# Kernel tuning notes

Measured on AMD Instinct MI355X. Metric: run time of the kernel, lower is better.

The kernel has to match this reference:

```python
import jax, jax.numpy as jnp
import numpy as np
import math

B, T, D, H = 128, 512, 512, 512


def setup_inputs() -> dict:
    key = jax.random.key(0)
    ks = jax.random.split(key, 6)
    s = 1.0 / math.sqrt(H)
    return {
        "values": jax.random.normal(ks[0], (B, T, D), jnp.float32),
        "Deltas": jax.random.uniform(ks[1], (B, T, D), jnp.float32),
        "W_att": jax.random.normal(ks[2], (D, D), jnp.float32) * s,
        "b_att": jnp.zeros((D,), jnp.float32),
        "W_ih": jax.random.normal(ks[3], (4 * H, D), jnp.float32) * s,
        "W_hh": jax.random.normal(ks[4], (4 * H, H), jnp.float32) * s,
        "b_ih": jnp.zeros((4 * H,), jnp.float32),
        "b_hh": jnp.zeros((4 * H,), jnp.float32),
    }


def lstm_cell(x, h, c, W_ih, W_hh, b_ih, b_hh):
    # torch.nn.LSTMCell: gates ordered i, f, g, o
    g = x @ W_ih.T + b_ih + h @ W_hh.T + b_hh
    i, f, gg, o = jnp.split(g, 4, axis=-1)
    c2 = jax.nn.sigmoid(f) * c + jax.nn.sigmoid(i) * jnp.tanh(gg)
    h2 = jax.nn.sigmoid(o) * jnp.tanh(c2)
    return h2, c2


def reference(values, Deltas, W_att, b_att, W_ih, W_hh, b_ih, b_hh):
    Bn, Tn, Dn = values.shape
    Hn = W_hh.shape[1]
    # cumsum over time then reverse along time (reverse_tensor)
    Del = jnp.flip(jnp.cumsum(Deltas, axis=-2), axis=1)  # [B,T,D]
    v_att = values @ W_att.T + b_att                      # attn-projected inputs [B,T,D]
    # a_ij = bmm(atten_linear(values), values^T) -> [B,T,T]
    a_ij = jnp.einsum('btd,bsd->bts', v_att, values)
    h0 = jnp.zeros((Bn, Hn), values.dtype)
    c0 = jnp.zeros((Bn, Hn), values.dtype)

    def step(carry, x_t):
        h, c = carry
        h2, c2 = lstm_cell(x_t, h, c, W_ih, W_hh, b_ih, b_hh)
        return (h2, c2), (h2, c2)

    xs = jnp.swapaxes(v_att[:, :-1], 0, 1)  # [T-1, B, D]
    (h_last, _), (hs, cs) = jax.lax.scan(step, (h0, c0), xs)
    hs = jnp.swapaxes(hs, 0, 1)  # [B, T-1, H]
    cs = jnp.swapaxes(cs, 0, 1)  # [B, T-1, H]

    # attention-weighted cell-state mixing for the final step
    alpha = jax.nn.softmax(a_ij[:, -1, :-1], axis=-1)[..., None]  # [B,T-1,1]
    d = Del[:, 1:]                                                # [B,T-1,D]
    C_i = jnp.sum(alpha * cs / jnp.log(math.e + d), axis=1)       # [B,H]

    hT, cT = lstm_cell(v_att[:, -1], h_last, C_i, W_ih, W_hh, b_ih, b_hh)
    h_n = jnp.concatenate([hs, hT[:, None, :]], axis=1)  # [B,T,H]
    return h_n
```

## Files before the change

kernel.cpp:

```cpp
#include <hip/hip_runtime.h>
#include <cstdint>

#define DEVI __device__ __forceinline__

typedef unsigned short ushort_t;
typedef __attribute__((ext_vector_type(8))) short s16x8;
typedef __attribute__((ext_vector_type(4))) int i32x4;
typedef __attribute__((ext_vector_type(4))) float f32x4;

DEVI ushort_t f2bf(float f) {
  uint32_t u = __builtin_bit_cast(uint32_t, f);
  u += 0x7fffu + ((u >> 16) & 1u);
  return (ushort_t)(u >> 16);
}
DEVI float bf2f(ushort_t u) {
  uint32_t x = ((uint32_t)u) << 16;
  return __builtin_bit_cast(float, x);
}
DEVI float sigmoidf_(float x) { return 1.0f / (1.0f + __expf(-x)); }
DEVI float tanhf_(float x) {
  float e = __expf(-2.0f * fabsf(x));
  float r = (1.0f - e) / (1.0f + e);
  return copysignf(r, x);
}

DEVI void load_tag16(i32x4& dst, const uint32_t* p) {
  asm volatile("global_load_dwordx4 %0, %1, off sc0 sc1" : "=v"(dst) : "v"(p));
}
DEVI void store_tagged(uint32_t* p, uint32_t v) {
  asm volatile("global_store_dword %0, %1, off sc0 sc1" :: "v"(p), "v"(v) : "memory");
}
DEVI void wait_vm0() { asm volatile("s_waitcnt vmcnt(0)" ::: "memory"); }

__global__ void cast_kernel(const float* __restrict__ in, ushort_t* __restrict__ out, long n) {
  long i = ((long)blockIdx.x * blockDim.x + threadIdx.x) * 8;
  if (i >= n) return;
  float4 a = *(const float4*)(in + i);
  float4 b = *(const float4*)(in + i + 4);
  union { s16x8 v; ushort_t u[8]; } r;
  r.u[0] = f2bf(a.x); r.u[1] = f2bf(a.y); r.u[2] = f2bf(a.z); r.u[3] = f2bf(a.w);
  r.u[4] = f2bf(b.x); r.u[5] = f2bf(b.y); r.u[6] = f2bf(b.z); r.u[7] = f2bf(b.w);
  *(s16x8*)(out + i) = r.v;
}

__global__ void transpose512(const float* __restrict__ in, float* __restrict__ out) {
  __shared__ float tile[32][33];
  int bx = blockIdx.x * 32, by = blockIdx.y * 32;
  int tx = threadIdx.x, ty = threadIdx.y;
  for (int i = 0; i < 32; i += 8)
    tile[ty + i][tx] = in[(by + ty + i) * 512 + bx + tx];
  __syncthreads();
  for (int i = 0; i < 32; i += 8)
    out[(bx + ty + i) * 512 + by + tx] = tile[tx][ty + i];
}

__global__ __launch_bounds__(256, 2)
void gemm_bt(const ushort_t* __restrict__ A, const ushort_t* __restrict__ B,
             const float* __restrict__ bias0, const float* __restrict__ bias1,
             ushort_t* __restrict__ C, int N, int K) {
  __shared__ __align__(16) ushort_t As[128 * 64];
  __shared__ __align__(16) ushort_t Bs[128 * 64];
  const int tid = threadIdx.x;
  const int lane = tid & 63, wv = tid >> 6;
  const int wm = wv >> 1, wn = wv & 1;
  const int l15 = lane & 15, l4 = lane >> 4;
  const long m0 = (long)blockIdx.x * 128;
  const int n0 = blockIdx.y * 128;
  const int nkt = K / 64;

  f32x4 acc[4][4] = {};

  int soff[4];
#pragma unroll
  for (int i = 0; i < 4; ++i) {
    int c = tid + i * 256;
    int r = c >> 3, ks = c & 7;
    soff[i] = r * 64 + ((ks ^ (r & 7)) << 3);
  }

#pragma unroll
  for (int i = 0; i < 4; ++i) {
    int c = tid + i * 256; int r = c >> 3; int ks = c & 7;
    *(s16x8*)&As[soff[i]] = *(const s16x8*)&A[(m0 + r) * K + ks * 8];
    *(s16x8*)&Bs[soff[i]] = *(const s16x8*)&B[(long)(n0 + r) * K + ks * 8];
  }
  __syncthreads();

  for (int kt = 0; kt < nkt; ++kt) {
    s16x8 ra[4], rb[4];
    const bool more = (kt + 1 < nkt);
    if (more) {
      const long kb = (long)(kt + 1) * 64;
#pragma unroll
      for (int i = 0; i < 4; ++i) {
        int c = tid + i * 256; int r = c >> 3; int ks = c & 7;
        ra[i] = *(const s16x8*)&A[(m0 + r) * K + kb + ks * 8];
        rb[i] = *(const s16x8*)&B[(long)(n0 + r) * K + kb + ks * 8];
      }
    }
#pragma unroll
    for (int kk = 0; kk < 2; ++kk) {
      s16x8 af[4], bfv[4];
      int slot = kk * 4 + l4;
#pragma unroll
      for (int i = 0; i < 4; ++i) {
        int rA = wm * 64 + i * 16 + l15;
        af[i] = *(const s16x8*)&As[rA * 64 + ((slot ^ (rA & 7)) << 3)];
        int rB = wn * 64 + i * 16 + l15;
        bfv[i] = *(const s16x8*)&Bs[rB * 64 + ((slot ^ (rB & 7)) << 3)];
      }
#pragma unroll
      for (int i = 0; i < 4; ++i)
#pragma unroll
        for (int j = 0; j < 4; ++j)
          acc[i][j] = __builtin_amdgcn_mfma_f32_16x16x32_bf16(af[i], bfv[j], acc[i][j], 0, 0, 0);
    }
    __syncthreads();
    if (more) {
#pragma unroll
      for (int i = 0; i < 4; ++i) {
        *(s16x8*)&As[soff[i]] = ra[i];
        *(s16x8*)&Bs[soff[i]] = rb[i];
      }
      __syncthreads();
    }
  }
#pragma unroll
  for (int i = 0; i < 4; ++i) {
#pragma unroll
    for (int j = 0; j < 4; ++j) {
#pragma unroll
      for (int r = 0; r < 4; ++r) {
        long m = m0 + wm * 64 + i * 16 + l4 * 4 + r;
        int n = n0 + wn * 64 + j * 16 + l15;
        float v = acc[i][j][r];
        if (bias0) v += bias0[n];
        if (bias1) v += bias1[n];
        C[m * (long)N + n] = f2bf(v);
      }
    }
  }
}

__global__ void bias_combo_kernel(const float* __restrict__ W_ih, const float* __restrict__ b_att,
                                  const float* __restrict__ b_ih, const float* __restrict__ b_hh,
                                  float* __restrict__ bc) {
  int n = blockIdx.x * 256 + threadIdx.x;
  __shared__ float ba[512];
  for (int k = threadIdx.x; k < 512; k += 256) ba[k] = b_att[k];
  __syncthreads();
  float s = b_ih[n] + b_hh[n];
  const float* row = W_ih + (long)n * 512;
  for (int k = 0; k < 512; ++k) s += row[k] * ba[k];
  bc[n] = s;
}

__global__ void vT_kernel(const float* __restrict__ values, const float* __restrict__ W_attT,
                          const float* __restrict__ b_att, float* __restrict__ vT) {
  int b = blockIdx.y;
  int n = blockIdx.x * 256 + threadIdx.x;
  __shared__ float xr[512];
  const float* row = values + ((long)b * 512 + 511) * 512;
  for (int k = threadIdx.x; k < 512; k += 256) xr[k] = row[k];
  __syncthreads();
  float acc = b_att[n];
  for (int k = 0; k < 512; ++k) acc += xr[k] * W_attT[k * 512 + n];
  vT[b * 512 + n] = acc;
}

__global__ void dtot_kernel(const float* __restrict__ Deltas, float* __restrict__ Dtot) {
  int idx = blockIdx.x * 256 + threadIdx.x;
  int b = idx >> 9, ch = idx & 511;
  const float* p = Deltas + (long)b * 512 * 512 + ch;
  float s = 0.0f;
  for (int t = 0; t < 511; ++t) s += p[(long)t * 512];
  Dtot[idx] = s;
}

__global__ void logits_kernel(const float* __restrict__ values, const float* __restrict__ vT,
                              float* __restrict__ logits) {
  int b = blockIdx.y;
  int wave = threadIdx.x >> 6, lane = threadIdx.x & 63;
  float vreg[8];
  const float* vtb = vT + b * 512;
#pragma unroll
  for (int j = 0; j < 8; ++j) vreg[j] = vtb[lane * 8 + j];
  int s0 = blockIdx.x * 64 + wave * 16;
  for (int si = 0; si < 16; ++si) {
    int s = s0 + si;
    if (s >= 511) break;
    const float* row = values + ((long)b * 512 + s) * 512 + lane * 8;
    float4 a = *(const float4*)row;
    float4 c = *(const float4*)(row + 4);
    float d = a.x * vreg[0] + a.y * vreg[1] + a.z * vreg[2] + a.w * vreg[3] +
              c.x * vreg[4] + c.y * vreg[5] + c.z * vreg[6] + c.w * vreg[7];
#pragma unroll
    for (int off = 32; off; off >>= 1) d += __shfl_xor(d, off);
    if (lane == 0) logits[b * 512 + s] = d;
  }
}

__global__ void softmax_kernel(float* __restrict__ logits) {
  int b = blockIdx.x, tid = threadIdx.x;
  __shared__ float wmax[4], wsum[4];
  float v0 = (tid < 511) ? logits[b * 512 + tid] : -1e30f;
  float v1 = (tid + 256 < 511) ? logits[b * 512 + tid + 256] : -1e30f;
  float m = fmaxf(v0, v1);
#pragma unroll
  for (int off = 32; off; off >>= 1) m = fmaxf(m, __shfl_xor(m, off));
  if ((tid & 63) == 0) wmax[tid >> 6] = m;
  __syncthreads();
  m = fmaxf(fmaxf(wmax[0], wmax[1]), fmaxf(wmax[2], wmax[3]));
  float e0 = (tid < 511) ? __expf(v0 - m) : 0.0f;
  float e1 = (tid + 256 < 511) ? __expf(v1 - m) : 0.0f;
  float s = e0 + e1;
#pragma unroll
  for (int off = 32; off; off >>= 1) s += __shfl_xor(s, off);
  if ((tid & 63) == 0) wsum[tid >> 6] = s;
  __syncthreads();
  s = wsum[0] + wsum[1] + wsum[2] + wsum[3];
  float inv = 1.0f / s;
  __syncthreads();
  if (tid < 511) logits[b * 512 + tid] = e0 * inv;
  if (tid + 256 < 511) logits[b * 512 + tid + 256] = e1 * inv;
}

__global__ __launch_bounds__(256, 1)
void scan_kernel(const float* __restrict__ W_hh, const ushort_t* __restrict__ Gx,
                 const float* __restrict__ alpha, const float* __restrict__ Dtot,
                 const float* __restrict__ Deltas, uint32_t* __restrict__ hbuf32,
                 float* __restrict__ out) {
  __shared__ __align__(16) ushort_t whh[64 * 512];
  __shared__ float gbuf[2][4][4][16][16];
  const int tid = threadIdx.x;
  const int bg = blockIdx.x & 7, hc = blockIdx.x >> 3;
  const int b0 = bg * 16, n0 = hc * 16;
  const int lane = tid & 63, wv = tid >> 6;
  const int l15 = lane & 15, l4 = lane >> 4;
  const int eb = tid >> 4, eh = tid & 15;
  const int bglob = b0 + eb, hglob = n0 + eh;

  for (int idx = tid; idx < 64 * 512; idx += 256) {
    int r = idx >> 9, k = idx & 511;
    int grow = (r >> 4) * 512 + n0 + (r & 15);
    float v = W_hh[(long)grow * 512 + k];
    int off = r * 512 + ((((k >> 3) ^ (r & 7)) << 3) | (k & 7));
    whh[off] = f2bf(v);
  }
  float c_state = 0.0f, Cacc = 0.0f;
  float running = Dtot[bglob * 512 + hglob];
  __syncthreads();

  s16x8 bfr[4][4];
#pragma unroll
  for (int g = 0; g < 4; ++g) {
    const int brow = g * 16 + l15;
#pragma unroll
    for (int kk4 = 0; kk4 < 4; ++kk4) {
      int ks = wv * 128 + kk4 * 32 + l4 * 8;
      int slot = (ks >> 3) ^ (brow & 7);
      bfr[g][kk4] = *(const s16x8*)&whh[brow * 512 + (slot << 3)];
    }
  }

  for (int t = 0; t < 512; ++t) {
    float a_t = 0.0f, delta_t = 0.0f;
    if (t < 511) {
      a_t = alpha[bglob * 512 + t];
      delta_t = Deltas[((long)bglob * 512 + (510 - t)) * 512 + hglob];
    }
    float gxv[4];
#pragma unroll
    for (int g = 0; g < 4; ++g)
      gxv[g] = bf2f(Gx[((long)bglob * 512 + t) * 2048 + g * 512 + hglob]);

    const uint32_t* hb = hbuf32 + ((t & 1) * 8 + bg) * 8192 + l15 * 512 + wv * 128 + l4 * 8;
    const uint32_t expect = (uint32_t)t << 16;
    i32x4 q[8];
    int guard = 0;
    for (;;) {
#pragma unroll
      for (int kk4 = 0; kk4 < 4; ++kk4) {
        load_tag16(q[kk4 * 2], hb + kk4 * 32);
        load_tag16(q[kk4 * 2 + 1], hb + kk4 * 32 + 4);
      }
      wait_vm0();
      __builtin_amdgcn_sched_barrier(0);
      uint32_t bad = 0;
#pragma unroll
      for (int i = 0; i < 8; ++i) {
        bad |= (uint32_t)q[i][0] ^ expect;
        bad |= (uint32_t)q[i][1] ^ expect;
        bad |= (uint32_t)q[i][2] ^ expect;
        bad |= (uint32_t)q[i][3] ^ expect;
      }
      if (!__any((bad & 0xffff0000u) != 0)) break;
      __builtin_amdgcn_s_sleep(1);
      if (++guard > (1 << 16)) break;
    }
    s16x8 afr[4];
#pragma unroll
    for (int kk4 = 0; kk4 < 4; ++kk4) {
#pragma unroll
      for (int j = 0; j < 4; ++j) {
        afr[kk4][j]     = (short)((uint32_t)q[kk4 * 2][j] & 0xffffu);
        afr[kk4][j + 4] = (short)((uint32_t)q[kk4 * 2 + 1][j] & 0xffffu);
      }
    }
    f32x4 acc[4] = {};
#pragma unroll
    for (int kk4 = 0; kk4 < 4; ++kk4)
#pragma unroll
      for (int g = 0; g < 4; ++g)
        acc[g] = __builtin_amdgcn_mfma_f32_16x16x32_bf16(afr[kk4], bfr[g][kk4], acc[g], 0, 0, 0);

    const int p = t & 1;
#pragma unroll
    for (int g = 0; g < 4; ++g)
#pragma unroll
      for (int r = 0; r < 4; ++r)
        gbuf[p][wv][g][l4 * 4 + r][l15] = acc[g][r];
    __syncthreads();

    float gate[4];
#pragma unroll
    for (int g = 0; g < 4; ++g)
      gate[g] = gbuf[p][0][g][eb][eh] + gbuf[p][1][g][eb][eh] +
                gbuf[p][2][g][eb][eh] + gbuf[p][3][g][eb][eh] + gxv[g];

    float cin = (t == 511) ? Cacc : c_state;
    float cnew = sigmoidf_(gate[1]) * cin + sigmoidf_(gate[0]) * tanhf_(gate[2]);
    float hnew = sigmoidf_(gate[3]) * tanhf_(cnew);
    out[((long)bglob * 512 + t) * 512 + hglob] = hnew;
    if (t < 511) {
      c_state = cnew;
      float rl = 1.0f / __logf(2.71828182845904523f + running);
      Cacc += a_t * cnew * rl;
      running -= delta_t;
      uint32_t w = ((uint32_t)(t + 1) << 16) | (uint32_t)f2bf(hnew);
      store_tagged(hbuf32 + (((t + 1) & 1) * 8 + bg) * 8192 + eb * 512 + hglob, w);
    }
  }
}

extern "C" void kernel_launch(void* const* d_in, const int* in_sizes, int n_in,
                              void* d_out, int out_size, void* d_ws, size_t ws_size,
                              hipStream_t stream) {
  const float* values = (const float*)d_in[0];
  const float* Deltas = (const float*)d_in[1];
  const float* W_att  = (const float*)d_in[2];
  const float* b_att  = (const float*)d_in[3];
  const float* W_ih   = (const float*)d_in[4];
  const float* W_hh   = (const float*)d_in[5];
  const float* b_ih   = (const float*)d_in[6];
  const float* b_hh   = (const float*)d_in[7];
  float* out = (float*)d_out;

  char* ws = (char*)d_ws;
  size_t off = 0;
  auto alloc = [&](size_t bytes) -> void* {
    void* p = ws + off;
    off += (bytes + 255) & ~(size_t)255;
    return p;
  };
  ushort_t* values_bf = (ushort_t*)alloc(67108864ull);
  ushort_t* Gx        = (ushort_t*)alloc(268435456ull);
  ushort_t* W_ih_bf   = (ushort_t*)alloc(2097152ull);
  ushort_t* Wc_bf     = (ushort_t*)alloc(2097152ull);
  float*    W_attT    = (float*)alloc(1048576ull);
  ushort_t* W_attT_bf = (ushort_t*)alloc(524288ull);
  float*    vT        = (float*)alloc(262144ull);
  float*    Dtot      = (float*)alloc(262144ull);
  float*    alpha     = (float*)alloc(262144ull);
  float*    bias_c    = (float*)alloc(8192ull);
  uint32_t* hbuf32    = (uint32_t*)alloc(524288ull);

  hipMemsetAsync(hbuf32, 0, 524288ull, stream);

  cast_kernel<<<33554432 / 8 / 256, 256, 0, stream>>>(values, values_bf, 33554432L);
  cast_kernel<<<1048576 / 8 / 256, 256, 0, stream>>>(W_ih, W_ih_bf, 1048576L);
  transpose512<<<dim3(16, 16), dim3(32, 8), 0, stream>>>(W_att, W_attT);
  cast_kernel<<<262144 / 8 / 256, 256, 0, stream>>>(W_attT, W_attT_bf, 262144L);

  gemm_bt<<<dim3(16, 4), 256, 0, stream>>>(W_ih_bf, W_attT_bf, nullptr, nullptr,
                                           Wc_bf, 512, 512);
  bias_combo_kernel<<<8, 256, 0, stream>>>(W_ih, b_att, b_ih, b_hh, bias_c);

  gemm_bt<<<dim3(512, 16), 256, 0, stream>>>(values_bf, Wc_bf, bias_c, nullptr,
                                             Gx, 2048, 512);

  vT_kernel<<<dim3(2, 128), 256, 0, stream>>>(values, W_attT, b_att, vT);
  dtot_kernel<<<256, 256, 0, stream>>>(Deltas, Dtot);
  logits_kernel<<<dim3(8, 128), 256, 0, stream>>>(values, vT, alpha);
  softmax_kernel<<<128, 256, 0, stream>>>(alpha);

  scan_kernel<<<256, 256, 0, stream>>>(W_hh, Gx, alpha, Dtot, Deltas, hbuf32, out);
}
```

Before: 2.285 ms.

## Poll hidden-state exchange through L2 with periodic system-scope fallback buffer

```diff
diff --git a/kernel.cpp b/kernel.cpp
--- a/kernel.cpp
+++ b/kernel.cpp
@@ -24,10 +24,16 @@
   return copysignf(r, x);
 }
 
-DEVI void load_tag16(i32x4& dst, const uint32_t* p) {
+DEVI void load_l2x4(i32x4& dst, const uint32_t* p) {
+  asm volatile("global_load_dwordx4 %0, %1, off sc0" : "=v"(dst) : "v"(p));
+}
+DEVI void load_mallx4(i32x4& dst, const uint32_t* p) {
   asm volatile("global_load_dwordx4 %0, %1, off sc0 sc1" : "=v"(dst) : "v"(p));
 }
-DEVI void store_tagged(uint32_t* p, uint32_t v) {
+DEVI void store_plain(uint32_t* p, uint32_t v) {
+  asm volatile("global_store_dword %0, %1, off" :: "v"(p), "v"(v) : "memory");
+}
+DEVI void store_mall(uint32_t* p, uint32_t v) {
   asm volatile("global_store_dword %0, %1, off sc0 sc1" :: "v"(p), "v"(v) : "memory");
 }
 DEVI void wait_vm0() { asm volatile("s_waitcnt vmcnt(0)" ::: "memory"); }
@@ -228,10 +234,10 @@
 __global__ __launch_bounds__(256, 1)
 void scan_kernel(const float* __restrict__ W_hh, const ushort_t* __restrict__ Gx,
                  const float* __restrict__ alpha, const float* __restrict__ Dtot,
-                 const float* __restrict__ Deltas, uint32_t* __restrict__ hbuf32,
-                 float* __restrict__ out) {
+                 const float* __restrict__ Deltas, uint32_t* __restrict__ hbufL2,
+                 uint32_t* __restrict__ hbufMALL, float* __restrict__ out) {
   __shared__ __align__(16) ushort_t whh[64 * 512];
-  __shared__ float gbuf[2][4][4][16][16];
+  __shared__ float gbuf[2][4][4][16][20];
   const int tid = threadIdx.x;
   const int bg = blockIdx.x & 7, hc = blockIdx.x >> 3;
   const int b0 = bg * 16, n0 = hc * 16;
@@ -273,16 +279,27 @@
 #pragma unroll
     for (int g = 0; g < 4; ++g)
       gxv[g] = bf2f(Gx[((long)bglob * 512 + t) * 2048 + g * 512 + hglob]);
-
-    const uint32_t* hb = hbuf32 + ((t & 1) * 8 + bg) * 8192 + l15 * 512 + wv * 128 + l4 * 8;
+    float rl = 1.0f / __logf(2.71828182845904523f + running);
+
+    const uint32_t base = ((t & 1) * 8 + bg) * 8192 + l15 * 512 + wv * 128 + l4 * 8;
+    const uint32_t* hb2 = hbufL2 + base;
+    const uint32_t* hbm = hbufMALL + base;
     const uint32_t expect = (uint32_t)t << 16;
     i32x4 q[8];
-    int guard = 0;
-    for (;;) {
-#pragma unroll
-      for (int kk4 = 0; kk4 < 4; ++kk4) {
-        load_tag16(q[kk4 * 2], hb + kk4 * 32);
-        load_tag16(q[kk4 * 2 + 1], hb + kk4 * 32 + 4);
+    bool got = false;
+    for (int guard = 0; !got && guard < (1 << 15); ++guard) {
+      if ((guard & 3) != 3) {
+#pragma unroll
+        for (int kk4 = 0; kk4 < 4; ++kk4) {
+          load_l2x4(q[kk4 * 2], hb2 + kk4 * 32);
+          load_l2x4(q[kk4 * 2 + 1], hb2 + kk4 * 32 + 4);
+        }
+      } else {
+#pragma unroll
+        for (int kk4 = 0; kk4 < 4; ++kk4) {
+          load_mallx4(q[kk4 * 2], hbm + kk4 * 32);
+          load_mallx4(q[kk4 * 2 + 1], hbm + kk4 * 32 + 4);
+        }
       }
       wait_vm0();
       __builtin_amdgcn_sched_barrier(0);
@@ -294,9 +311,7 @@
         bad |= (uint32_t)q[i][2] ^ expect;
         bad |= (uint32_t)q[i][3] ^ expect;
       }
-      if (!__any((bad & 0xffff0000u) != 0)) break;
-      __builtin_amdgcn_s_sleep(1);
-      if (++guard > (1 << 16)) break;
+      got = !__any((bad & 0xffff0000u) != 0);
     }
     s16x8 afr[4];
 #pragma unroll
@@ -331,14 +346,17 @@
     float cin = (t == 511) ? Cacc : c_state;
     float cnew = sigmoidf_(gate[1]) * cin + sigmoidf_(gate[0]) * tanhf_(gate[2]);
     float hnew = sigmoidf_(gate[3]) * tanhf_(cnew);
+    if (t < 511) {
+      uint32_t w = ((uint32_t)(t + 1) << 16) | (uint32_t)f2bf(hnew);
+      uint32_t widx = (((t + 1) & 1) * 8 + bg) * 8192 + eb * 512 + hglob;
+      store_plain(hbufL2 + widx, w);
+      store_mall(hbufMALL + widx, w);
+    }
     out[((long)bglob * 512 + t) * 512 + hglob] = hnew;
     if (t < 511) {
       c_state = cnew;
-      float rl = 1.0f / __logf(2.71828182845904523f + running);
       Cacc += a_t * cnew * rl;
       running -= delta_t;
-      uint32_t w = ((uint32_t)(t + 1) << 16) | (uint32_t)f2bf(hnew);
-      store_tagged(hbuf32 + (((t + 1) & 1) * 8 + bg) * 8192 + eb * 512 + hglob, w);
     }
   }
 }
@@ -373,9 +391,10 @@
   float*    Dtot      = (float*)alloc(262144ull);
   float*    alpha     = (float*)alloc(262144ull);
   float*    bias_c    = (float*)alloc(8192ull);
-  uint32_t* hbuf32    = (uint32_t*)alloc(524288ull);
-
-  hipMemsetAsync(hbuf32, 0, 524288ull, stream);
+  uint32_t* hbufL2    = (uint32_t*)alloc(524288ull);
+  uint32_t* hbufMALL  = (uint32_t*)alloc(524288ull);
+
+  hipMemsetAsync(hbufL2, 0, 1048576ull, stream);
 
   cast_kernel<<<33554432 / 8 / 256, 256, 0, stream>>>(values, values_bf, 33554432L);
   cast_kernel<<<1048576 / 8 / 256, 256, 0, stream>>>(W_ih, W_ih_bf, 1048576L);
@@ -394,5 +413,5 @@
   logits_kernel<<<dim3(8, 128), 256, 0, stream>>>(values, vT, alpha);
   softmax_kernel<<<128, 256, 0, stream>>>(alpha);
 
-  scan_kernel<<<256, 256, 0, stream>>>(W_hh, Gx, alpha, Dtot, Deltas, hbuf32, out);
-}
+  scan_kernel<<<256, 256, 0, stream>>>(W_hh, Gx, alpha, Dtot, Deltas, hbufL2, hbufMALL, out);
+}
```

Result: slower. 2.489 ms (+8.9%).

## Halve scan grid with 512-thread blocks covering 32 hidden columns each

Applied to the files above, without the earlier changes.

```diff
diff --git a/kernel.cpp b/kernel.cpp
--- a/kernel.cpp
+++ b/kernel.cpp
@@ -24,10 +24,10 @@
   return copysignf(r, x);
 }
 
-DEVI void load_tag16(i32x4& dst, const uint32_t* p) {
+DEVI void load_mallx4(i32x4& dst, const uint32_t* p) {
   asm volatile("global_load_dwordx4 %0, %1, off sc0 sc1" : "=v"(dst) : "v"(p));
 }
-DEVI void store_tagged(uint32_t* p, uint32_t v) {
+DEVI void store_mall(uint32_t* p, uint32_t v) {
   asm volatile("global_store_dword %0, %1, off sc0 sc1" :: "v"(p), "v"(v) : "memory");
 }
 DEVI void wait_vm0() { asm volatile("s_waitcnt vmcnt(0)" ::: "memory"); }
@@ -225,24 +225,25 @@
   if (tid + 256 < 511) logits[b * 512 + tid + 256] = e1 * inv;
 }
 
-__global__ __launch_bounds__(256, 1)
+__global__ __launch_bounds__(512, 1)
 void scan_kernel(const float* __restrict__ W_hh, const ushort_t* __restrict__ Gx,
                  const float* __restrict__ alpha, const float* __restrict__ Dtot,
                  const float* __restrict__ Deltas, uint32_t* __restrict__ hbuf32,
                  float* __restrict__ out) {
-  __shared__ __align__(16) ushort_t whh[64 * 512];
-  __shared__ float gbuf[2][4][4][16][16];
+  __shared__ __align__(16) ushort_t whh[128 * 512];
+  float* gbufF = (float*)whh;
   const int tid = threadIdx.x;
   const int bg = blockIdx.x & 7, hc = blockIdx.x >> 3;
-  const int b0 = bg * 16, n0 = hc * 16;
+  const int b0 = bg * 16, n0 = hc * 32;
   const int lane = tid & 63, wv = tid >> 6;
+  const int ks = wv & 3, hcol = wv >> 2;
   const int l15 = lane & 15, l4 = lane >> 4;
-  const int eb = tid >> 4, eh = tid & 15;
+  const int eb = tid >> 5, eh = tid & 31;
   const int bglob = b0 + eb, hglob = n0 + eh;
 
-  for (int idx = tid; idx < 64 * 512; idx += 256) {
+  for (int idx = tid; idx < 128 * 512; idx += 512) {
     int r = idx >> 9, k = idx & 511;
-    int grow = (r >> 4) * 512 + n0 + (r & 15);
+    int grow = (r >> 5) * 512 + n0 + ((r >> 4) & 1) * 16 + (r & 15);
     float v = W_hh[(long)grow * 512 + k];
     int off = r * 512 + ((((k >> 3) ^ (r & 7)) << 3) | (k & 7));
     whh[off] = f2bf(v);
@@ -254,35 +255,49 @@
   s16x8 bfr[4][4];
 #pragma unroll
   for (int g = 0; g < 4; ++g) {
-    const int brow = g * 16 + l15;
+    const int brow = g * 32 + hcol * 16 + l15;
 #pragma unroll
     for (int kk4 = 0; kk4 < 4; ++kk4) {
-      int ks = wv * 128 + kk4 * 32 + l4 * 8;
-      int slot = (ks >> 3) ^ (brow & 7);
+      int k = ks * 128 + kk4 * 32 + l4 * 8;
+      int slot = (k >> 3) ^ (brow & 7);
       bfr[g][kk4] = *(const s16x8*)&whh[brow * 512 + (slot << 3)];
     }
   }
+  __syncthreads();
+
+  const uint32_t pollOff = (uint32_t)(l15 * 512 + ks * 128 + l4 * 8);
+  const uint32_t wOff = (uint32_t)(eb * 512 + hglob);
+  uint32_t* slab[2] = { hbuf32 + bg * 8192, hbuf32 + (8 + bg) * 8192 };
+  const ushort_t* gxbase = Gx + (long)bglob * 512 * 2048 + hglob;
+  const float* dbase = Deltas + (long)bglob * 512 * 512 + hglob;
+  const float* abase = alpha + bglob * 512;
+  float* obase = out + (long)bglob * 512 * 512 + hglob;
+
+  auto GIDX = [](int h2, int k4, int g, int row, int col) {
+    return (((h2 * 4 + k4) * 4 + g) * 16 + row) * 18 + col;
+  };
 
   for (int t = 0; t < 512; ++t) {
     float a_t = 0.0f, delta_t = 0.0f;
     if (t < 511) {
-      a_t = alpha[bglob * 512 + t];
-      delta_t = Deltas[((long)bglob * 512 + (510 - t)) * 512 + hglob];
-    }
-    float gxv[4];
+      a_t = abase[t];
+      delta_t = dbase[(long)(510 - t) * 512];
+    }
+    ushort_t gxr[4];
 #pragma unroll
     for (int g = 0; g < 4; ++g)
-      gxv[g] = bf2f(Gx[((long)bglob * 512 + t) * 2048 + g * 512 + hglob]);
-
-    const uint32_t* hb = hbuf32 + ((t & 1) * 8 + bg) * 8192 + l15 * 512 + wv * 128 + l4 * 8;
+      gxr[g] = gxbase[(long)t * 2048 + g * 512];
+    float rl = 1.0f / __logf(2.71828182845904523f + running);
+
+    const uint32_t* pb = slab[t & 1] + pollOff;
     const uint32_t expect = (uint32_t)t << 16;
     i32x4 q[8];
-    int guard = 0;
+    int sweeps = 0;
     for (;;) {
 #pragma unroll
-      for (int kk4 = 0; kk4 < 4; ++kk4) {
-        load_tag16(q[kk4 * 2], hb + kk4 * 32);
-        load_tag16(q[kk4 * 2 + 1], hb + kk4 * 32 + 4);
+      for (int k = 0; k < 4; ++k) {
+        load_mallx4(q[k * 2], pb + k * 32);
+        load_mallx4(q[k * 2 + 1], pb + k * 32 + 4);
       }
       wait_vm0();
       __builtin_amdgcn_sched_barrier(0);
@@ -295,17 +310,22 @@
         bad |= (uint32_t)q[i][3] ^ expect;
       }
       if (!__any((bad & 0xffff0000u) != 0)) break;
-      __builtin_amdgcn_s_sleep(1);
-      if (++guard > (1 << 16)) break;
+      if (++sweeps > (1 << 15)) break;
+      if (sweeps > 2) {
+        __builtin_amdgcn_s_sleep(4);
+      } else {
+        __builtin_amdgcn_s_sleep(1);
+      }
     }
     s16x8 afr[4];
 #pragma unroll
     for (int kk4 = 0; kk4 < 4; ++kk4) {
-#pragma unroll
-      for (int j = 0; j < 4; ++j) {
-        afr[kk4][j]     = (short)((uint32_t)q[kk4 * 2][j] & 0xffffu);
-        afr[kk4][j + 4] = (short)((uint32_t)q[kk4 * 2 + 1][j] & 0xffffu);
-      }
+      union { uint32_t d[4]; s16x8 v; } u;
+      u.d[0] = __builtin_amdgcn_perm((uint32_t)q[kk4 * 2][1], (uint32_t)q[kk4 * 2][0], 0x05040100u);
+      u.d[1] = __builtin_amdgcn_perm((uint32_t)q[kk4 * 2][3], (uint32_t)q[kk4 * 2][2], 0x05040100u);
+      u.d[2] = __builtin_amdgcn_perm((uint32_t)q[kk4 * 2 + 1][1], (uint32_t)q[kk4 * 2 + 1][0], 0x05040100u);
+      u.d[3] = __builtin_amdgcn_perm((uint32_t)q[kk4 * 2 + 1][3], (uint32_t)q[kk4 * 2 + 1][2], 0x05040100u);
+      afr[kk4] = u.v;
     }
     f32x4 acc[4] = {};
 #pragma unroll
@@ -314,31 +334,34 @@
       for (int g = 0; g < 4; ++g)
         acc[g] = __builtin_amdgcn_mfma_f32_16x16x32_bf16(afr[kk4], bfr[g][kk4], acc[g], 0, 0, 0);
 
-    const int p = t & 1;
 #pragma unroll
     for (int g = 0; g < 4; ++g)
 #pragma unroll
       for (int r = 0; r < 4; ++r)
-        gbuf[p][wv][g][l4 * 4 + r][l15] = acc[g][r];
+        gbufF[GIDX(hcol, ks, g, l4 * 4 + r, l15)] = acc[g][r];
     __syncthreads();
 
+    const int hr = eh >> 4, col = eh & 15;
     float gate[4];
 #pragma unroll
     for (int g = 0; g < 4; ++g)
-      gate[g] = gbuf[p][0][g][eb][eh] + gbuf[p][1][g][eb][eh] +
-                gbuf[p][2][g][eb][eh] + gbuf[p][3][g][eb][eh] + gxv[g];
+      gate[g] = gbufF[GIDX(hr, 0, g, eb, col)] + gbufF[GIDX(hr, 1, g, eb, col)] +
+                gbufF[GIDX(hr, 2, g, eb, col)] + gbufF[GIDX(hr, 3, g, eb, col)] + bf2f(gxr[g]);
+    __syncthreads();
 
     float cin = (t == 511) ? Cacc : c_state;
     float cnew = sigmoidf_(gate[1]) * cin + sigmoidf_(gate[0]) * tanhf_(gate[2]);
     float hnew = sigmoidf_(gate[3]) * tanhf_(cnew);
-    out[((long)bglob * 512 + t) * 512 + hglob] = hnew;
+
     if (t < 511) {
+      uint32_t w = ((uint32_t)(t + 1) << 16) | (uint32_t)f2bf(hnew);
+      store_mall(slab[(t + 1) & 1] + wOff, w);
+      obase[(long)t * 512] = hnew;
       c_state = cnew;
-      float rl = 1.0f / __logf(2.71828182845904523f + running);
       Cacc += a_t * cnew * rl;
       running -= delta_t;
-      uint32_t w = ((uint32_t)(t + 1) << 16) | (uint32_t)f2bf(hnew);
-      store_tagged(hbuf32 + (((t + 1) & 1) * 8 + bg) * 8192 + eb * 512 + hglob, w);
+    } else {
+      obase[(long)t * 512] = hnew;
     }
   }
 }
@@ -375,7 +398,7 @@
   float*    bias_c    = (float*)alloc(8192ull);
   uint32_t* hbuf32    = (uint32_t*)alloc(524288ull);
 
-  hipMemsetAsync(hbuf32, 0, 524288ull, stream);
+  (void)hipMemsetAsync(hbuf32, 0, 524288ull, stream);
 
   cast_kernel<<<33554432 / 8 / 256, 256, 0, stream>>>(values, values_bf, 33554432L);
   cast_kernel<<<1048576 / 8 / 256, 256, 0, stream>>>(W_ih, W_ih_bf, 1048576L);
@@ -394,5 +417,5 @@
   logits_kernel<<<dim3(8, 128), 256, 0, stream>>>(values, vT, alpha);
   softmax_kernel<<<128, 256, 0, stream>>>(alpha);
 
-  scan_kernel<<<256, 256, 0, stream>>>(W_hh, Gx, alpha, Dtot, Deltas, hbuf32, out);
-}
+  scan_kernel<<<128, 512, 0, stream>>>(W_hh, Gx, alpha, Dtot, Deltas, hbuf32, out);
+}
```

New measurement: 2.715 ms. 1.19x slower.
